# Optimization experiments

Hardware: AMD Instinct MI355X
Metric: run time of the kernel (lower is better)

The kernel has to match this reference:

```python
import jax, jax.numpy as jnp
import numpy as np
import math

B, H, N, D = 2, 16, 2048, 64

def setup_inputs() -> dict:
    key = jax.random.key(0)
    kq, kk, kv, kb = jax.random.split(key, 4)
    return {
        "query": jax.random.normal(kq, (B, H, N, D), dtype=jnp.float32),
        "key": jax.random.normal(kk, (B, H, N, D), dtype=jnp.float32),
        "value": jax.random.normal(kv, (B, H, N, D), dtype=jnp.float32),
        "relative_position_bias": jax.random.normal(kb, (H, N, N), dtype=jnp.float32),
    }

def reference(query, key, value, relative_position_bias):
    d = query.shape[-1]
    # scores: [B,H,N,N]
    attn = jnp.einsum("bhnd,bhmd->bhnm", query, key) / jnp.sqrt(jnp.asarray(d, query.dtype))
    attn = attn + relative_position_bias[None]  # broadcast over batch
    attn = jax.nn.softmax(attn, axis=-1)
    # dropout p=0.0 -> identity
    output = jnp.einsum("bhnm,bhmd->bhnd", attn, value)
    return (output, attn)
```

## Files before the change

kernel.cpp:

```cpp
#include <hip/hip_runtime.h>
#include <cstdint>

#define BN 2
#define HN 16
#define NN 2048
#define DD 64
#define KT 64
#define NT (NN / KT)
#define QB 128
#define LDP 72
#define LDF 68

typedef __attribute__((ext_vector_type(8))) short short8;
typedef __attribute__((ext_vector_type(2))) uint32_t uint2v;
typedef __attribute__((ext_vector_type(4))) uint32_t uint4v;
typedef __attribute__((ext_vector_type(4))) float float4v;

static __device__ __forceinline__ uint32_t cvt_pk_bf16(float a, float b){
    uint32_t r;
    asm("v_cvt_pk_bf16_f32 %0, %1, %2" : "=v"(r) : "v"(a), "v"(b));
    return r;
}
static __device__ __forceinline__ unsigned short f2bf1(float a){
    return (unsigned short)(cvt_pk_bf16(a, a) & 0xffffu);
}
static __device__ __forceinline__ short8 pack8(float4v f0, float4v f1){
    uint4v u;
    u[0] = cvt_pk_bf16(f0[0], f0[1]);
    u[1] = cvt_pk_bf16(f0[2], f0[3]);
    u[2] = cvt_pk_bf16(f1[0], f1[1]);
    u[3] = cvt_pk_bf16(f1[2], f1[3]);
    return __builtin_bit_cast(short8, u);
}

static __device__ __forceinline__ float4v mfma_bf16(short8 a, short8 b, float4v c){
    return __builtin_amdgcn_mfma_f32_16x16x32_bf16(a, b, c, 0, 0, 0);
}

static __device__ __forceinline__ void barrier_lds(){
    asm volatile("s_waitcnt lgkmcnt(0)" ::: "memory");
    __builtin_amdgcn_s_barrier();
    asm volatile("" ::: "memory");
}
static __device__ __forceinline__ void lgkm_drain(){
    asm volatile("s_waitcnt lgkmcnt(0)" ::: "memory");
}

__launch_bounds__(512, 4)
__global__ void attn_fused_kernel(const float* __restrict__ Q,
                                  const float* __restrict__ K,
                                  const float* __restrict__ V,
                                  const float* __restrict__ Bias,
                                  float* __restrict__ Out){
    __shared__ unsigned short Kb[2][KT][LDP];
    __shared__ unsigned short Vt[2][DD][LDP];
    __shared__ float Pb[8][16][LDF];

    const int raw  = blockIdx.x;
    const int slot = raw & 7;
    const int idx  = raw >> 3;
    const int h    = slot * 2 + (idx >> 5);
    const int rem  = idx & 31;
    const int b    = rem & 1;
    const int rt   = rem >> 1;

    const int tid = threadIdx.x;
    const int l   = tid & 63;
    const int w   = tid >> 6;
    const int lg  = l >> 4;
    const int ll  = l & 15;
    const int vc  = ll * 4;

    const int srow = tid >> 4;
    const int scol = (tid & 15) << 2;
    const int vsw  = ((tid >> 1) & 7) << 3;

    const int qw = rt * QB + w * 16;
    const size_t bh = (size_t)(b * HN + h);
    const float* Qg = Q + (bh * NN + qw) * DD;
    const float* Kg = K + bh * NN * DD;
    const float* Vg = V + bh * NN * DD;
    const float* BgV = Bias + (size_t)h * NN * NN + (size_t)(qw + lg) * NN + vc;

    short8 qf[2];
    {
        const float* qrow = Qg + (size_t)ll * DD + lg * 8;
        #pragma unroll
        for(int ks = 0; ks < 2; ++ks)
            qf[ks] = pack8(*(const float4v*)(qrow + ks * 32),
                           *(const float4v*)(qrow + ks * 32 + 4));
    }

    float lsum[4];
    #pragma unroll
    for(int r = 0; r < 4; ++r) lsum[r] = 0.f;

    float4v kreg[2], bv[4];
    #pragma unroll
    for(int i = 0; i < 2; ++i)
        kreg[i] = *(const float4v*)(Kg + (size_t)(srow + 32*i) * DD + scol);
    #pragma unroll
    for(int i = 0; i < 2; ++i){
        uint2v t = { cvt_pk_bf16(kreg[i][0], kreg[i][1]),
                     cvt_pk_bf16(kreg[i][2], kreg[i][3]) };
        *(uint2v*)&Kb[0][srow + 32*i][scol] = t;
    }
    #pragma unroll
    for(int i = 0; i < 2; ++i)
        kreg[i] = *(const float4v*)(Kg + (size_t)(KT + srow + 32*i) * DD + scol);
    #pragma unroll
    for(int it = 0; it < 4; ++it)
        bv[it] = *(const float4v*)(BgV + (size_t)(it * 4) * NN);
    barrier_lds();

    for(int ct = 0; ct < NT; ++ct){
        const int cur = ct & 1;
        if(ct + 1 < NT){
            #pragma unroll
            for(int i = 0; i < 2; ++i){
                uint2v t = { cvt_pk_bf16(kreg[i][0], kreg[i][1]),
                             cvt_pk_bf16(kreg[i][2], kreg[i][3]) };
                *(uint2v*)&Kb[cur ^ 1][srow + 32*i][scol] = t;
            }
        }
        if(ct + 2 < NT){
            #pragma unroll
            for(int i = 0; i < 2; ++i)
                kreg[i] = *(const float4v*)(Kg + (size_t)((ct+2)*KT + srow + 32*i) * DD + scol);
        }
        #pragma unroll
        for(int it = 0; it < 4; ++it)
            *(float4v*)&Pb[w][it*4 + lg][vc] = bv[it];
        if(ct + 1 < NT){
            #pragma unroll
            for(int it = 0; it < 4; ++it)
                bv[it] = *(const float4v*)(BgV + (size_t)(it * 4) * NN + (ct+1)*KT);
        }

        float4v acc[4];
        #pragma unroll
        for(int sub = 0; sub < 4; ++sub) acc[sub] = (float4v){0.f,0.f,0.f,0.f};
        __builtin_amdgcn_s_setprio(1);
        #pragma unroll
        for(int sub = 0; sub < 4; ++sub){
            short8 b0 = *(const short8*)&Kb[cur][sub*16 + ll][lg*8];
            short8 b1 = *(const short8*)&Kb[cur][sub*16 + ll][32 + lg*8];
            acc[sub] = mfma_bf16(qf[0], b0, acc[sub]);
            acc[sub] = mfma_bf16(qf[1], b1, acc[sub]);
        }
        __builtin_amdgcn_s_setprio(0);

        #pragma unroll
        for(int r = 0; r < 4; ++r){
            float e0 = __expf(acc[0][r] * 0.125f + Pb[w][lg*4+r][      ll]);
            float e1 = __expf(acc[1][r] * 0.125f + Pb[w][lg*4+r][16 +  ll]);
            float e2 = __expf(acc[2][r] * 0.125f + Pb[w][lg*4+r][32 +  ll]);
            float e3 = __expf(acc[3][r] * 0.125f + Pb[w][lg*4+r][48 +  ll]);
            lsum[r] += (e0 + e1) + (e2 + e3);
        }
        barrier_lds();
    }

    float rl[4];
    #pragma unroll
    for(int r = 0; r < 4; ++r){
        #pragma unroll
        for(int d = 1; d < 16; d <<= 1) lsum[r] += __shfl_xor(lsum[r], d);
        rl[r] = 1.0f / lsum[r];
    }

    float4v oacc[4];
    #pragma unroll
    for(int ds = 0; ds < 4; ++ds) oacc[ds] = (float4v){0.f,0.f,0.f,0.f};

    float* attnW = Out + (size_t)BN*HN*NN*DD
                 + (bh * NN + qw + lg) * (size_t)NN + vc;

    float4v vreg[2];
    #pragma unroll
    for(int i = 0; i < 2; ++i){
        kreg[i] = *(const float4v*)(Kg + (size_t)(srow + 32*i) * DD + scol);
        vreg[i] = *(const float4v*)(Vg + (size_t)(srow + 32*i) * DD + scol);
    }
    #pragma unroll
    for(int i = 0; i < 2; ++i){
        uint2v t = { cvt_pk_bf16(kreg[i][0], kreg[i][1]),
                     cvt_pk_bf16(kreg[i][2], kreg[i][3]) };
        *(uint2v*)&Kb[0][srow + 32*i][scol] = t;
        #pragma unroll
        for(int j = 0; j < 4; ++j)
            Vt[0][scol + j][(srow + 32*i) ^ vsw] = f2bf1(vreg[i][j]);
    }
    #pragma unroll
    for(int i = 0; i < 2; ++i){
        kreg[i] = *(const float4v*)(Kg + (size_t)(KT + srow + 32*i) * DD + scol);
        vreg[i] = *(const float4v*)(Vg + (size_t)(KT + srow + 32*i) * DD + scol);
    }
    #pragma unroll
    for(int it = 0; it < 4; ++it)
        bv[it] = *(const float4v*)(BgV + (size_t)(it * 4) * NN);
    barrier_lds();

    for(int ct = 0; ct < NT; ++ct){
        const int cur = ct & 1;
        if(ct + 1 < NT){
            #pragma unroll
            for(int i = 0; i < 2; ++i){
                uint2v t = { cvt_pk_bf16(kreg[i][0], kreg[i][1]),
                             cvt_pk_bf16(kreg[i][2], kreg[i][3]) };
                *(uint2v*)&Kb[cur ^ 1][srow + 32*i][scol] = t;
                #pragma unroll
                for(int j = 0; j < 4; ++j)
                    Vt[cur ^ 1][scol + j][(srow + 32*i) ^ vsw] = f2bf1(vreg[i][j]);
            }
        }
        if(ct + 2 < NT){
            #pragma unroll
            for(int i = 0; i < 2; ++i){
                kreg[i] = *(const float4v*)(Kg + (size_t)((ct+2)*KT + srow + 32*i) * DD + scol);
                vreg[i] = *(const float4v*)(Vg + (size_t)((ct+2)*KT + srow + 32*i) * DD + scol);
            }
        }
        #pragma unroll
        for(int it = 0; it < 4; ++it)
            *(float4v*)&Pb[w][it*4 + lg][vc] = bv[it];
        if(ct + 1 < NT){
            #pragma unroll
            for(int it = 0; it < 4; ++it)
                bv[it] = *(const float4v*)(BgV + (size_t)(it * 4) * NN + (ct+1)*KT);
        }

        float4v acc[4];
        #pragma unroll
        for(int sub = 0; sub < 4; ++sub) acc[sub] = (float4v){0.f,0.f,0.f,0.f};
        __builtin_amdgcn_s_setprio(1);
        #pragma unroll
        for(int sub = 0; sub < 4; ++sub){
            short8 b0 = *(const short8*)&Kb[cur][sub*16 + ll][lg*8];
            short8 b1 = *(const short8*)&Kb[cur][sub*16 + ll][32 + lg*8];
            acc[sub] = mfma_bf16(qf[0], b0, acc[sub]);
            acc[sub] = mfma_bf16(qf[1], b1, acc[sub]);
        }
        __builtin_amdgcn_s_setprio(0);

        #pragma unroll
        for(int sub = 0; sub < 2; ++sub)
            #pragma unroll
            for(int r = 0; r < 4; ++r){
                float sv = acc[sub][r] * 0.125f + Pb[w][lg*4+r][sub*16+ll];
                Pb[w][lg*4+r][sub*16+ll] = __expf(sv) * rl[r];
            }
        lgkm_drain();

        short8 pf0;
        {
            float4v p0 = *(const float4v*)&Pb[w][ll][lg*8];
            float4v p1 = *(const float4v*)&Pb[w][ll][lg*8 + 4];
            pf0 = pack8(p0, p1);
        }
        #pragma unroll
        for(int sub = 2; sub < 4; ++sub)
            #pragma unroll
            for(int r = 0; r < 4; ++r){
                float sv = acc[sub][r] * 0.125f + Pb[w][lg*4+r][sub*16+ll];
                Pb[w][lg*4+r][sub*16+ll] = __expf(sv) * rl[r];
            }

        __builtin_amdgcn_s_setprio(1);
        #pragma unroll
        for(int ds = 0; ds < 4; ++ds){
            const int rsw = (2*ds + (ll >> 3)) << 3;
            short8 v0 = *(const short8*)&Vt[cur][ds*16 + ll][(lg*8) ^ rsw];
            oacc[ds] = mfma_bf16(pf0, v0, oacc[ds]);
        }
        __builtin_amdgcn_s_setprio(0);
        lgkm_drain();

        short8 pf1;
        {
            float4v p2 = *(const float4v*)&Pb[w][ll][32 + lg*8];
            float4v p3 = *(const float4v*)&Pb[w][ll][32 + lg*8 + 4];
            pf1 = pack8(p2, p3);
        }
        __builtin_amdgcn_s_setprio(1);
        #pragma unroll
        for(int ds = 0; ds < 4; ++ds){
            const int rsw = (2*ds + (ll >> 3)) << 3;
            short8 v1 = *(const short8*)&Vt[cur][ds*16 + ll][(32 + lg*8) ^ rsw];
            oacc[ds] = mfma_bf16(pf1, v1, oacc[ds]);
        }
        __builtin_amdgcn_s_setprio(0);

        #pragma unroll
        for(int it = 0; it < 4; ++it){
            float4v pv = *(const float4v*)&Pb[w][it*4 + lg][vc];
            *(float4v*)(attnW + (size_t)(it*4) * NN + ct*KT) = pv;
        }

        barrier_lds();
    }

    float* outG = Out + (bh * NN + qw) * (size_t)DD;
    #pragma unroll
    for(int ds = 0; ds < 4; ++ds)
        #pragma unroll
        for(int r = 0; r < 4; ++r)
            outG[(size_t)(lg*4 + r) * DD + ds*16 + ll] = oacc[ds][r];
}

extern "C" void kernel_launch(void* const* d_in, const int* in_sizes, int n_in,
                              void* d_out, int out_size, void* d_ws, size_t ws_size,
                              hipStream_t stream) {
    const float* q    = (const float*)d_in[0];
    const float* k    = (const float*)d_in[1];
    const float* v    = (const float*)d_in[2];
    const float* bias = (const float*)d_in[3];
    float* out = (float*)d_out;

    dim3 grid(BN * HN * (NN / QB));
    dim3 block(512);
    hipLaunchKernelGGL(attn_fused_kernel, grid, block, 0, stream, q, k, v, bias, out);
}
```

Baseline: 287.4 us.

## Pre-transpose V to bf16 in workspace and load MFMA operands directly from global

Adds a separate kernel that converts V to bf16 and stores it transposed in the workspace. The attention kernel then reads V fragments straight from global/L2 into registers and no longer stages V through LDS. This removes the per-tile V conversion, the scattered LDS transpose stores and the Vt LDS buffer. The cost is an extra kernel launch and workspace traffic, plus uncoalesced-ish per-wave global loads of V that are repeated by every block sharing the same head.

```diff
diff --git a/kernel.cpp b/kernel.cpp
--- a/kernel.cpp
+++ b/kernel.cpp
@@ -10,6 +10,7 @@
 #define QB 128
 #define LDP 72
 #define LDF 68
+#define KVELEMS ((size_t)BN * HN * NN * DD)
 
 typedef __attribute__((ext_vector_type(8))) short short8;
 typedef __attribute__((ext_vector_type(2))) uint32_t uint2v;
@@ -46,14 +47,41 @@
     asm volatile("s_waitcnt lgkmcnt(0)" ::: "memory");
 }
 
+__global__ void transpose_v_kernel(const float* __restrict__ V,
+                                   unsigned short* __restrict__ VTW){
+    __shared__ unsigned short T[64][72];
+    const int bid = blockIdx.x;
+    const int bh  = bid >> 5;
+    const int ct  = bid & 31;
+    const int tid = threadIdx.x;
+
+    const float* src = V + ((size_t)bh * NN + ct * 64) * DD;
+    const int srow = tid >> 4;
+    const int scol = (tid & 15) << 2;
+    #pragma unroll
+    for(int i = 0; i < 4; ++i){
+        const int row = srow + 16 * i;
+        float4v f = *(const float4v*)(src + (size_t)row * DD + scol);
+        #pragma unroll
+        for(int j = 0; j < 4; ++j)
+            T[scol + j][row] = f2bf1(f[j]);
+    }
+    __syncthreads();
+    unsigned short* dst = VTW + (size_t)bh * DD * NN + ct * 64;
+    const int d  = tid >> 2;
+    const int kc = (tid & 3) << 4;
+    *(uint4v*)(dst + (size_t)d * NN + kc)     = *(const uint4v*)&T[d][kc];
+    *(uint4v*)(dst + (size_t)d * NN + kc + 8) = *(const uint4v*)&T[d][kc + 8];
+}
+
 __launch_bounds__(512, 4)
 __global__ void attn_fused_kernel(const float* __restrict__ Q,
                                   const float* __restrict__ K,
                                   const float* __restrict__ V,
                                   const float* __restrict__ Bias,
+                                  const unsigned short* __restrict__ VTW,
                                   float* __restrict__ Out){
     __shared__ unsigned short Kb[2][KT][LDP];
-    __shared__ unsigned short Vt[2][DD][LDP];
     __shared__ float Pb[8][16][LDF];
 
     const int raw  = blockIdx.x;
@@ -73,13 +101,12 @@
 
     const int srow = tid >> 4;
     const int scol = (tid & 15) << 2;
-    const int vsw  = ((tid >> 1) & 7) << 3;
 
     const int qw = rt * QB + w * 16;
     const size_t bh = (size_t)(b * HN + h);
     const float* Qg = Q + (bh * NN + qw) * DD;
     const float* Kg = K + bh * NN * DD;
-    const float* Vg = V + bh * NN * DD;
+    const unsigned short* vtF = VTW + bh * DD * NN + (size_t)ll * NN + lg * 8;
     const float* BgV = Bias + (size_t)h * NN * NN + (size_t)(qw + lg) * NN + vc;
 
     short8 qf[2];
@@ -176,26 +203,18 @@
     float* attnW = Out + (size_t)BN*HN*NN*DD
                  + (bh * NN + qw + lg) * (size_t)NN + vc;
 
-    float4v vreg[2];
-    #pragma unroll
-    for(int i = 0; i < 2; ++i){
+    #pragma unroll
+    for(int i = 0; i < 2; ++i)
         kreg[i] = *(const float4v*)(Kg + (size_t)(srow + 32*i) * DD + scol);
-        vreg[i] = *(const float4v*)(Vg + (size_t)(srow + 32*i) * DD + scol);
-    }
     #pragma unroll
     for(int i = 0; i < 2; ++i){
         uint2v t = { cvt_pk_bf16(kreg[i][0], kreg[i][1]),
                      cvt_pk_bf16(kreg[i][2], kreg[i][3]) };
         *(uint2v*)&Kb[0][srow + 32*i][scol] = t;
-        #pragma unroll
-        for(int j = 0; j < 4; ++j)
-            Vt[0][scol + j][(srow + 32*i) ^ vsw] = f2bf1(vreg[i][j]);
-    }
-    #pragma unroll
-    for(int i = 0; i < 2; ++i){
+    }
+    #pragma unroll
+    for(int i = 0; i < 2; ++i)
         kreg[i] = *(const float4v*)(Kg + (size_t)(KT + srow + 32*i) * DD + scol);
-        vreg[i] = *(const float4v*)(Vg + (size_t)(KT + srow + 32*i) * DD + scol);
-    }
     #pragma unroll
     for(int it = 0; it < 4; ++it)
         bv[it] = *(const float4v*)(BgV + (size_t)(it * 4) * NN);
@@ -209,17 +228,12 @@
                 uint2v t = { cvt_pk_bf16(kreg[i][0], kreg[i][1]),
                              cvt_pk_bf16(kreg[i][2], kreg[i][3]) };
                 *(uint2v*)&Kb[cur ^ 1][srow + 32*i][scol] = t;
-                #pragma unroll
-                for(int j = 0; j < 4; ++j)
-                    Vt[cur ^ 1][scol + j][(srow + 32*i) ^ vsw] = f2bf1(vreg[i][j]);
             }
         }
         if(ct + 2 < NT){
             #pragma unroll
-            for(int i = 0; i < 2; ++i){
+            for(int i = 0; i < 2; ++i)
                 kreg[i] = *(const float4v*)(Kg + (size_t)((ct+2)*KT + srow + 32*i) * DD + scol);
-                vreg[i] = *(const float4v*)(Vg + (size_t)((ct+2)*KT + srow + 32*i) * DD + scol);
-            }
         }
         #pragma unroll
         for(int it = 0; it < 4; ++it)
@@ -229,6 +243,14 @@
             for(int it = 0; it < 4; ++it)
                 bv[it] = *(const float4v*)(BgV + (size_t)(it * 4) * NN + (ct+1)*KT);
         }
+
+        short8 vf[8];
+        #pragma unroll
+        for(int ds = 0; ds < 4; ++ds)
+            #pragma unroll
+            for(int ks = 0; ks < 2; ++ks)
+                vf[ds*2+ks] = __builtin_bit_cast(short8,
+                    *(const uint4v*)(vtF + (size_t)(ds*16) * NN + ct*KT + ks*32));
 
         float4v acc[4];
         #pragma unroll
@@ -268,11 +290,8 @@
 
         __builtin_amdgcn_s_setprio(1);
         #pragma unroll
-        for(int ds = 0; ds < 4; ++ds){
-            const int rsw = (2*ds + (ll >> 3)) << 3;
-            short8 v0 = *(const short8*)&Vt[cur][ds*16 + ll][(lg*8) ^ rsw];
-            oacc[ds] = mfma_bf16(pf0, v0, oacc[ds]);
-        }
+        for(int ds = 0; ds < 4; ++ds)
+            oacc[ds] = mfma_bf16(pf0, vf[ds*2+0], oacc[ds]);
         __builtin_amdgcn_s_setprio(0);
         lgkm_drain();
 
@@ -284,11 +303,8 @@
         }
         __builtin_amdgcn_s_setprio(1);
         #pragma unroll
-        for(int ds = 0; ds < 4; ++ds){
-            const int rsw = (2*ds + (ll >> 3)) << 3;
-            short8 v1 = *(const short8*)&Vt[cur][ds*16 + ll][(32 + lg*8) ^ rsw];
-            oacc[ds] = mfma_bf16(pf1, v1, oacc[ds]);
-        }
+        for(int ds = 0; ds < 4; ++ds)
+            oacc[ds] = mfma_bf16(pf1, vf[ds*2+1], oacc[ds]);
         __builtin_amdgcn_s_setprio(0);
 
         #pragma unroll
@@ -316,8 +332,10 @@
     const float* v    = (const float*)d_in[2];
     const float* bias = (const float*)d_in[3];
     float* out = (float*)d_out;
-
-    dim3 grid(BN * HN * (NN / QB));
-    dim3 block(512);
-    hipLaunchKernelGGL(attn_fused_kernel, grid, block, 0, stream, q, k, v, bias, out);
-}
+    unsigned short* vtw = (unsigned short*)d_ws;
+
+    hipLaunchKernelGGL(transpose_v_kernel, dim3(BN * HN * (NN / 64)), dim3(256), 0, stream,
+                       v, vtw);
+    hipLaunchKernelGGL(attn_fused_kernel, dim3(BN * HN * (NN / QB)), dim3(512), 0, stream,
+                       q, k, v, bias, vtw, out);
+}
```

Measured after the change: 344.5 us. +19.8%, slower.
